# Performance work log

Hardware: AMD Instinct MI355X
Metric: run time of the kernel (lower is better)

Reference implementation:

```python
import jax, jax.numpy as jnp
import numpy as np

D = 1024  # repr_dims


def setup_inputs() -> dict:
    key = jax.random.key(0)
    ks = jax.random.split(key, 10)
    B, T = 32, 2048
    inp = {
        "raw_residual": jax.random.normal(ks[0], (B, T, D), jnp.float32),
        "rel_residual": jax.random.normal(ks[1], (B, T, D), jnp.float32),
        "raw_global": jax.random.normal(ks[2], (B, D), jnp.float32),
        "spec_global": jax.random.normal(ks[3], (B, D), jnp.float32),
        "relation_global": jax.random.normal(ks[4], (B, D), jnp.float32),
        # LayerNorm(3D) params
        "ln_gamma": jnp.ones((3 * D,), jnp.float32),
        "ln_beta": jnp.zeros((3 * D,), jnp.float32),
        # Linear(3D -> D)
        "w1": jax.random.normal(ks[5], (3 * D, D), jnp.float32) * (1.0 / np.sqrt(3 * D)),
        "b1": jnp.zeros((D,), jnp.float32),
        # Linear(D -> 1), bias init -2.1972246 per module
        "w2": jax.random.normal(ks[6], (D, 1), jnp.float32) * (1.0 / np.sqrt(D)),
        "b2": jnp.full((1,), -2.1972246, jnp.float32),
    }
    return inp


def reference(raw_residual, rel_residual, raw_global, spec_global, relation_global,
              ln_gamma, ln_beta, w1, b1, w2, b2):
    # Concatenate globals: [B, 3D]
    g = jnp.concatenate([raw_global, spec_global, relation_global], axis=-1)
    # LayerNorm (eps=1e-5, like torch default)
    mu = jnp.mean(g, axis=-1, keepdims=True)
    var = jnp.mean(jnp.square(g - mu), axis=-1, keepdims=True)
    g = (g - mu) * jax.lax.rsqrt(var + 1e-5) * ln_gamma + ln_beta
    # 2-layer MLP gate with exact (erf) GELU, then sigmoid -> alpha [B, 1]
    h = jax.nn.gelu(g @ w1 + b1, approximate=False)
    alpha = jax.nn.sigmoid(h @ w2 + b2)
    # Scaled residual add: alpha broadcast over the sequence axis (dim 1)
    main_repr = raw_residual + alpha[:, None, :] * rel_residual
    return main_repr, alpha
```

## Files before the change

### kernel.cpp

```cpp
#include <hip/hip_runtime.h>
#include <math.h>

#define D_ 1024
#define THREE_D 3072
#define B_ 32
#define T_ 2048

typedef float floatx4 __attribute__((ext_vector_type(4)));

__global__ __launch_bounds__(256) void ln_kernel(
    const float* __restrict__ raw_g, const float* __restrict__ spec_g,
    const float* __restrict__ rel_g, const float* __restrict__ gamma,
    const float* __restrict__ beta, float* __restrict__ gnT,
    float* __restrict__ pre_alpha) {
  const int b = blockIdx.x;
  const int tid = threadIdx.x;
  __shared__ float sg[THREE_D];
  __shared__ float red[8];
  __shared__ float stats[2];

  if (tid == 0) pre_alpha[b] = 0.f;

  float s = 0.f, s2 = 0.f;
#pragma unroll
  for (int i = 0; i < 12; ++i) {
    int k = i * 256 + tid;
    float v;
    if (k < 1024)       v = raw_g[b * 1024 + k];
    else if (k < 2048)  v = spec_g[b * 1024 + (k - 1024)];
    else                v = rel_g[b * 1024 + (k - 2048)];
    sg[k] = v;
    s += v;
    s2 += v * v;
  }
#pragma unroll
  for (int off = 32; off; off >>= 1) {
    s  += __shfl_down(s, off, 64);
    s2 += __shfl_down(s2, off, 64);
  }
  const int wv = tid >> 6;
  if ((tid & 63) == 0) { red[wv] = s; red[4 + wv] = s2; }
  __syncthreads();
  if (tid == 0) {
    float ts  = red[0] + red[1] + red[2] + red[3];
    float ts2 = red[4] + red[5] + red[6] + red[7];
    float mu  = ts * (1.0f / THREE_D);
    float var = ts2 * (1.0f / THREE_D) - mu * mu;
    stats[0] = mu;
    stats[1] = rsqrtf(var + 1e-5f);
  }
  __syncthreads();
  const float mu = stats[0], rstd = stats[1];
#pragma unroll
  for (int i = 0; i < 12; ++i) {
    int k = i * 256 + tid;
    gnT[k * 32 + b] = (sg[k] - mu) * rstd * gamma[k] + beta[k];
  }
}

__global__ __launch_bounds__(512) void gate_gemm(
    const float* __restrict__ gnT, const float* __restrict__ w1,
    float* __restrict__ partials) {
  const int tid   = threadIdx.x;
  const int lane  = tid & 63;
  const int wvid  = tid >> 6;
  const int khalf = wvid >> 1;
  const int bhalf = wvid & 1;
  const int jt = blockIdx.x;
  const int by = blockIdx.y;
  const int j  = jt * 64 + lane;
  const int kslice = by * 4 + khalf;

  __shared__ float sg[192 * 32];
  const float* gsrc = gnT + by * 192 * 32;
#pragma unroll
  for (int i = 0; i < 12; ++i) sg[i * 512 + tid] = gsrc[i * 512 + tid];
  __syncthreads();

  const float* wrow = w1 + (size_t)kslice * 48 * D_ + j;
  float w[48];
#pragma unroll
  for (int kk = 0; kk < 48; ++kk) w[kk] = wrow[(size_t)kk * D_];

  float4 acc[4];
#pragma unroll
  for (int i = 0; i < 4; ++i) acc[i] = make_float4(0.f, 0.f, 0.f, 0.f);

  const float4* gp = (const float4*)(sg + (khalf * 48) * 32 + bhalf * 16);
#pragma unroll
  for (int kk = 0; kk < 48; ++kk) {
    const float4* g = gp + kk * 8;
    const float wv_ = w[kk];
#pragma unroll
    for (int i = 0; i < 4; ++i) {
      float4 gv = g[i];
      acc[i].x = fmaf(gv.x, wv_, acc[i].x);
      acc[i].y = fmaf(gv.y, wv_, acc[i].y);
      acc[i].z = fmaf(gv.z, wv_, acc[i].z);
      acc[i].w = fmaf(gv.w, wv_, acc[i].w);
    }
  }

  float* base = partials + ((size_t)(kslice * 2 + bhalf) * 16) * D_ + j;
#pragma unroll
  for (int i = 0; i < 4; ++i) {
    base[(4 * i + 0) * D_] = acc[i].x;
    base[(4 * i + 1) * D_] = acc[i].y;
    base[(4 * i + 2) * D_] = acc[i].z;
    base[(4 * i + 3) * D_] = acc[i].w;
  }
}

__global__ __launch_bounds__(256) void gate_finish(
    const float* __restrict__ partials, const float* __restrict__ b1,
    const float* __restrict__ w2, float* __restrict__ pre_alpha) {
  const int jc  = blockIdx.x;
  const int b   = blockIdx.y;
  const int tid = threadIdx.x;
  const int j   = jc * 256 + tid;
  const int bh  = b >> 4, br = b & 15;

  const float* p = partials + ((size_t)bh * 16 + br) * D_ + j;
  float s = b1[j];
#pragma unroll 8
  for (int sl = 0; sl < 64; ++sl)
    s += p[(size_t)sl * 32768];
  float h = 0.5f * s * (1.0f + erff(s * 0.7071067811865476f));
  float c = h * w2[j];

#pragma unroll
  for (int off = 32; off; off >>= 1) c += __shfl_down(c, off, 64);
  __shared__ float red[4];
  if ((tid & 63) == 0) red[tid >> 6] = c;
  __syncthreads();
  if (tid == 0)
    atomicAdd(&pre_alpha[b], red[0] + red[1] + red[2] + red[3]);
}

__global__ __launch_bounds__(64) void alphify(
    const float* __restrict__ pre_alpha, const float* __restrict__ b2,
    float* __restrict__ alpha_out) {
  const int tid = threadIdx.x;
  if (tid < B_) {
    float t = pre_alpha[tid] + b2[0];
    alpha_out[tid] = 1.0f / (1.0f + expf(-t));
  }
}

__global__ __launch_bounds__(256) void fuse_kernel(
    const float4* __restrict__ raw, const float4* __restrict__ rel,
    const float* __restrict__ alpha, float* __restrict__ out) {
  const int b = blockIdx.y;
  const float a = alpha[b];
  const size_t f4_per_b = (size_t)T_ * D_ / 4;
  const size_t base = (size_t)b * f4_per_b + (size_t)blockIdx.x * 1024 + threadIdx.x;

  float4 r0 = raw[base +   0], r1 = raw[base + 256],
         r2 = raw[base + 512], r3 = raw[base + 768];
  float4 e0 = rel[base +   0], e1 = rel[base + 256],
         e2 = rel[base + 512], e3 = rel[base + 768];

  floatx4 o0, o1, o2, o3;
  o0.x = fmaf(a, e0.x, r0.x); o0.y = fmaf(a, e0.y, r0.y);
  o0.z = fmaf(a, e0.z, r0.z); o0.w = fmaf(a, e0.w, r0.w);
  o1.x = fmaf(a, e1.x, r1.x); o1.y = fmaf(a, e1.y, r1.y);
  o1.z = fmaf(a, e1.z, r1.z); o1.w = fmaf(a, e1.w, r1.w);
  o2.x = fmaf(a, e2.x, r2.x); o2.y = fmaf(a, e2.y, r2.y);
  o2.z = fmaf(a, e2.z, r2.z); o2.w = fmaf(a, e2.w, r2.w);
  o3.x = fmaf(a, e3.x, r3.x); o3.y = fmaf(a, e3.y, r3.y);
  o3.z = fmaf(a, e3.z, r3.z); o3.w = fmaf(a, e3.w, r3.w);

  floatx4* o = reinterpret_cast<floatx4*>(out) + base;
  __builtin_nontemporal_store(o0, o +   0);
  __builtin_nontemporal_store(o1, o + 256);
  __builtin_nontemporal_store(o2, o + 512);
  __builtin_nontemporal_store(o3, o + 768);
}

extern "C" void kernel_launch(void* const* d_in, const int* in_sizes, int n_in,
                              void* d_out, int out_size, void* d_ws, size_t ws_size,
                              hipStream_t stream) {
  const float* raw_res = (const float*)d_in[0];
  const float* rel_res = (const float*)d_in[1];
  const float* raw_g   = (const float*)d_in[2];
  const float* spec_g  = (const float*)d_in[3];
  const float* rel_g   = (const float*)d_in[4];
  const float* gamma   = (const float*)d_in[5];
  const float* beta    = (const float*)d_in[6];
  const float* w1      = (const float*)d_in[7];
  const float* b1      = (const float*)d_in[8];
  const float* w2      = (const float*)d_in[9];
  const float* b2      = (const float*)d_in[10];

  float* out = (float*)d_out;
  float* gnT       = out;
  float* pre_alpha = out + 120000;
  float* partials  = out + 131072;
  float* alpha     = out + (size_t)B_ * T_ * D_;

  ln_kernel<<<dim3(B_), dim3(256), 0, stream>>>(raw_g, spec_g, rel_g, gamma, beta,
                                                gnT, pre_alpha);
  gate_gemm<<<dim3(16, 16), dim3(512), 0, stream>>>(gnT, w1, partials);
  gate_finish<<<dim3(4, B_), dim3(256), 0, stream>>>(partials, b1, w2, pre_alpha);
  alphify<<<dim3(1), dim3(64), 0, stream>>>(pre_alpha, b2, alpha);
  fuse_kernel<<<dim3(512, B_), dim3(256), 0, stream>>>(
      (const float4*)raw_res, (const float4*)rel_res, alpha, d_out ? (float*)d_out : nullptr);
}
```

Measured before the change: 626.8 us.

## Fold sigmoid into gate_finish via last-block counter and restructure fuse grid

Removes the separate alphify launch by having the last of the four gate_finish blocks per batch row (tracked with an atomic counter) compute the sigmoid. The fuse kernel now launches 2048 blocks that each loop over all 32 batch rows at a fixed position. It also switches from nontemporal to normal stores. This saves one kernel launch, but the new access pattern strides each thread across batches 8 MB apart, and dropping nontemporal stores may pollute the cache.

```diff
diff --git a/kernel.cpp b/kernel.cpp
--- a/kernel.cpp
+++ b/kernel.cpp
@@ -6,20 +6,18 @@
 #define B_ 32
 #define T_ 2048
 
-typedef float floatx4 __attribute__((ext_vector_type(4)));
-
 __global__ __launch_bounds__(256) void ln_kernel(
     const float* __restrict__ raw_g, const float* __restrict__ spec_g,
     const float* __restrict__ rel_g, const float* __restrict__ gamma,
     const float* __restrict__ beta, float* __restrict__ gnT,
-    float* __restrict__ pre_alpha) {
+    float* __restrict__ pre_alpha, int* __restrict__ cnt) {
   const int b = blockIdx.x;
   const int tid = threadIdx.x;
   __shared__ float sg[THREE_D];
   __shared__ float red[8];
   __shared__ float stats[2];
 
-  if (tid == 0) pre_alpha[b] = 0.f;
+  if (tid == 0) { pre_alpha[b] = 0.f; cnt[b] = 0; }
 
   float s = 0.f, s2 = 0.f;
 #pragma unroll
@@ -113,7 +111,9 @@
 
 __global__ __launch_bounds__(256) void gate_finish(
     const float* __restrict__ partials, const float* __restrict__ b1,
-    const float* __restrict__ w2, float* __restrict__ pre_alpha) {
+    const float* __restrict__ w2, const float* __restrict__ b2,
+    float* __restrict__ pre_alpha, int* __restrict__ cnt,
+    float* __restrict__ alpha_out) {
   const int jc  = blockIdx.x;
   const int b   = blockIdx.y;
   const int tid = threadIdx.x;
@@ -133,48 +133,50 @@
   __shared__ float red[4];
   if ((tid & 63) == 0) red[tid >> 6] = c;
   __syncthreads();
-  if (tid == 0)
+  if (tid == 0) {
     atomicAdd(&pre_alpha[b], red[0] + red[1] + red[2] + red[3]);
-}
-
-__global__ __launch_bounds__(64) void alphify(
-    const float* __restrict__ pre_alpha, const float* __restrict__ b2,
-    float* __restrict__ alpha_out) {
-  const int tid = threadIdx.x;
-  if (tid < B_) {
-    float t = pre_alpha[tid] + b2[0];
-    alpha_out[tid] = 1.0f / (1.0f + expf(-t));
+    __threadfence();
+    int old = atomicAdd(&cnt[b], 1);
+    if (old == 3) {
+      float tot = atomicAdd(&pre_alpha[b], 0.f) + b2[0];
+      alpha_out[b] = 1.0f / (1.0f + expf(-tot));
+    }
   }
 }
 
 __global__ __launch_bounds__(256) void fuse_kernel(
     const float4* __restrict__ raw, const float4* __restrict__ rel,
-    const float* __restrict__ alpha, float* __restrict__ out) {
-  const int b = blockIdx.y;
-  const float a = alpha[b];
-  const size_t f4_per_b = (size_t)T_ * D_ / 4;
-  const size_t base = (size_t)b * f4_per_b + (size_t)blockIdx.x * 1024 + threadIdx.x;
-
-  float4 r0 = raw[base +   0], r1 = raw[base + 256],
-         r2 = raw[base + 512], r3 = raw[base + 768];
-  float4 e0 = rel[base +   0], e1 = rel[base + 256],
-         e2 = rel[base + 512], e3 = rel[base + 768];
-
-  floatx4 o0, o1, o2, o3;
-  o0.x = fmaf(a, e0.x, r0.x); o0.y = fmaf(a, e0.y, r0.y);
-  o0.z = fmaf(a, e0.z, r0.z); o0.w = fmaf(a, e0.w, r0.w);
-  o1.x = fmaf(a, e1.x, r1.x); o1.y = fmaf(a, e1.y, r1.y);
-  o1.z = fmaf(a, e1.z, r1.z); o1.w = fmaf(a, e1.w, r1.w);
-  o2.x = fmaf(a, e2.x, r2.x); o2.y = fmaf(a, e2.y, r2.y);
-  o2.z = fmaf(a, e2.z, r2.z); o2.w = fmaf(a, e2.w, r2.w);
-  o3.x = fmaf(a, e3.x, r3.x); o3.y = fmaf(a, e3.y, r3.y);
-  o3.z = fmaf(a, e3.z, r3.z); o3.w = fmaf(a, e3.w, r3.w);
-
-  floatx4* o = reinterpret_cast<floatx4*>(out) + base;
-  __builtin_nontemporal_store(o0, o +   0);
-  __builtin_nontemporal_store(o1, o + 256);
-  __builtin_nontemporal_store(o2, o + 512);
-  __builtin_nontemporal_store(o3, o + 768);
+    const float* __restrict__ alpha, float4* __restrict__ out) {
+  const size_t tid0 = (size_t)blockIdx.x * 256 + threadIdx.x;
+  const size_t S = (size_t)T_ * D_ / 4;
+
+#pragma unroll
+  for (int s8 = 0; s8 < 8; ++s8) {
+    const int s = s8 * 4;
+    const size_t i0 = tid0 + (size_t)(s + 0) * S;
+    const size_t i1 = tid0 + (size_t)(s + 1) * S;
+    const size_t i2 = tid0 + (size_t)(s + 2) * S;
+    const size_t i3 = tid0 + (size_t)(s + 3) * S;
+    const float a0 = alpha[s + 0], a1 = alpha[s + 1];
+    const float a2 = alpha[s + 2], a3 = alpha[s + 3];
+
+    float4 r0 = raw[i0], e0 = rel[i0];
+    float4 r1 = raw[i1], e1 = rel[i1];
+    float4 r2 = raw[i2], e2 = rel[i2];
+    float4 r3 = raw[i3], e3 = rel[i3];
+
+    float4 o0, o1, o2, o3;
+    o0.x = fmaf(a0, e0.x, r0.x); o0.y = fmaf(a0, e0.y, r0.y);
+    o0.z = fmaf(a0, e0.z, r0.z); o0.w = fmaf(a0, e0.w, r0.w);
+    o1.x = fmaf(a1, e1.x, r1.x); o1.y = fmaf(a1, e1.y, r1.y);
+    o1.z = fmaf(a1, e1.z, r1.z); o1.w = fmaf(a1, e1.w, r1.w);
+    o2.x = fmaf(a2, e2.x, r2.x); o2.y = fmaf(a2, e2.y, r2.y);
+    o2.z = fmaf(a2, e2.z, r2.z); o2.w = fmaf(a2, e2.w, r2.w);
+    o3.x = fmaf(a3, e3.x, r3.x); o3.y = fmaf(a3, e3.y, r3.y);
+    o3.z = fmaf(a3, e3.z, r3.z); o3.w = fmaf(a3, e3.w, r3.w);
+
+    out[i0] = o0; out[i1] = o1; out[i2] = o2; out[i3] = o3;
+  }
 }
 
 extern "C" void kernel_launch(void* const* d_in, const int* in_sizes, int n_in,
@@ -194,15 +196,16 @@
 
   float* out = (float*)d_out;
   float* gnT       = out;
-  float* pre_alpha = out + 120000;
+  float* pre_alpha = out + 100000;
+  int*   cnt       = (int*)(out + 100064);
   float* partials  = out + 131072;
   float* alpha     = out + (size_t)B_ * T_ * D_;
 
   ln_kernel<<<dim3(B_), dim3(256), 0, stream>>>(raw_g, spec_g, rel_g, gamma, beta,
-                                                gnT, pre_alpha);
+                                                gnT, pre_alpha, cnt);
   gate_gemm<<<dim3(16, 16), dim3(512), 0, stream>>>(gnT, w1, partials);
-  gate_finish<<<dim3(4, B_), dim3(256), 0, stream>>>(partials, b1, w2, pre_alpha);
-  alphify<<<dim3(1), dim3(64), 0, stream>>>(pre_alpha, b2, alpha);
-  fuse_kernel<<<dim3(512, B_), dim3(256), 0, stream>>>(
-      (const float4*)raw_res, (const float4*)rel_res, alpha, d_out ? (float*)d_out : nullptr);
-}
+  gate_finish<<<dim3(4, B_), dim3(256), 0, stream>>>(partials, b1, w2, b2,
+                                                     pre_alpha, cnt, alpha);
+  fuse_kernel<<<dim3(2048), dim3(256), 0, stream>>>(
+      (const float4*)raw_res, (const float4*)rel_res, alpha, (float4*)d_out);
+}
```

Result: slower. 674.9 us (+7.7%).
